# Kernel optimization log

Measured on AMD Instinct MI355X. Metric: run time of the kernel, lower is better.

Reference implementation:

```python
import jax, jax.numpy as jnp
import numpy as np

CHEB_K = 3
HIDDEN = 64
HORIZON = 12
H_FSIZE = 64                      # conv kernel width along the hidden axis
H_FILTER = HORIZON * H_FSIZE      # 768, forced by h.view(N,1,horizon,1,h_filter_size)
N_NODE = 1024
BATCH = 64
T_IN = 12
K2 = (CHEB_K * HIDDEN) ** 2       # 36864, hyp Linear in_features


def setup_inputs() -> dict:
    key = jax.random.key(0)
    k1, k2, k3, k4 = jax.random.split(key, 4)
    output = jax.random.normal(k1, (BATCH, T_IN, N_NODE, HIDDEN), jnp.float32)
    weights = jax.random.normal(k2, (N_NODE, K2), jnp.float32)
    # hyp Linear parameters (torch default init scale ~ 1/sqrt(fan_in))
    W_hyp = jax.random.normal(k3, (H_FILTER, K2), jnp.float32) / np.sqrt(K2).astype(np.float32)
    b_hyp = jax.random.normal(k4, (H_FILTER,), jnp.float32) / np.sqrt(K2).astype(np.float32)
    return {"output": output, "weights": weights, "W_hyp": W_hyp, "b_hyp": b_hyp}


def reference(output, weights, W_hyp, b_hyp):
    B, T, N, D = output.shape
    x = output[:, -1]                              # (B, N, D)   last time step
    w = weights.reshape(N, -1)                     # (N, K2)
    h = w @ W_hyp.T + b_hyp                        # (N, h_filter) hypernet Linear
    h = h.reshape(N, HORIZON, H_FSIZE)             # per-node, per-horizon 1xF filters
    Wout = D - H_FSIZE + 1                         # valid conv width (=1 here)
    # sliding windows of x along D: (B, N, Wout, F)
    idx = jnp.arange(Wout)[:, None] + jnp.arange(H_FSIZE)[None, :]
    xw = x[:, :, idx]
    # grouped conv2d (groups=N, 1 in-ch / horizon out-ch per group) == per-node contraction.
    # The torch sum(dim=3) is over a size-1 axis (no-op). Final layout (B, horizon, N, Wout).
    out = jnp.einsum('bnwf,ntf->btnw', xw, h)
    return out
```

## Files before the change

kernel.cpp:

```cpp
#include <hip/hip_runtime.h>
#include <hip/hip_bf16.h>
#include <cstdint>
#include <cstddef>

#define K2V 36864
#define MN  1024
#define HF  768

typedef __attribute__((ext_vector_type(8))) short short8;
typedef __attribute__((ext_vector_type(4))) float f32x4;

__device__ __forceinline__ unsigned pk_bf2(float a, float b) {
    __hip_bfloat16 ha = __float2bfloat16(a);
    __hip_bfloat16 hb = __float2bfloat16(b);
    unsigned short ua = *reinterpret_cast<unsigned short*>(&ha);
    unsigned short ub = *reinterpret_cast<unsigned short*>(&hb);
    return (unsigned)ua | ((unsigned)ub << 16);
}

__global__ __launch_bounds__(512, 4)
void gemm_h_split(const float* __restrict__ A, const float* __restrict__ B,
                  float* __restrict__ part, int KC)
{
    __shared__ unsigned short sA[2][128 * 64];
    __shared__ unsigned short sB[2][128 * 64];

    const int tid  = threadIdx.x;
    const int lane = tid & 63;
    const int wave = tid >> 6;
    const int wm   = wave >> 2;
    const int wn   = wave & 3;

    int mtile, ntile, kidx;
    if ((gridDim.x & 7) == 0) {
        const int xcd = blockIdx.x & 7;
        const int pos = blockIdx.x >> 3;
        mtile = xcd;
        kidx  = pos / 6;
        ntile = pos - kidx * 6;
    } else {
        kidx = blockIdx.x / 48;
        const int rem = blockIdx.x - kidx * 48;
        mtile = rem / 6;
        ntile = rem - mtile * 6;
    }
    const int k0 = kidx * KC;

    const float* Ap = A + (size_t)(mtile * 128) * K2V + k0;
    const float* Bp = B + (size_t)(ntile * 128) * K2V + k0;

    const int c4 = tid & 15;
    const int r0 = tid >> 4;

    f32x4 acc[4][2];
    #pragma unroll
    for (int i = 0; i < 4; ++i)
        #pragma unroll
        for (int j = 0; j < 2; ++j)
            acc[i][j] = (f32x4){0.f, 0.f, 0.f, 0.f};

    float4 ra[4], rb[4];

    auto load_step = [&](int s) {
        const float* a = Ap + s * 64 + c4 * 4;
        const float* b = Bp + s * 64 + c4 * 4;
        #pragma unroll
        for (int i = 0; i < 4; ++i) {
            const int r = r0 + 32 * i;
            ra[i] = *reinterpret_cast<const float4*>(a + (size_t)r * K2V);
            rb[i] = *reinterpret_cast<const float4*>(b + (size_t)r * K2V);
        }
    };
    auto write_step = [&](int buf) {
        #pragma unroll
        for (int i = 0; i < 4; ++i) {
            const int r = r0 + 32 * i;
            int off = r * 128 + c4 * 8;
            off ^= (r & 7) << 4;
            uint2 va = { pk_bf2(ra[i].x, ra[i].y), pk_bf2(ra[i].z, ra[i].w) };
            uint2 vb = { pk_bf2(rb[i].x, rb[i].y), pk_bf2(rb[i].z, rb[i].w) };
            *reinterpret_cast<uint2*>(reinterpret_cast<char*>(sA[buf]) + off) = va;
            *reinterpret_cast<uint2*>(reinterpret_cast<char*>(sB[buf]) + off) = vb;
        }
    };

    const int nsteps = KC >> 6;

    load_step(0);
    write_step(0);
    __syncthreads();

    for (int s = 0; s < nsteps; ++s) {
        if (s + 1 < nsteps) load_step(s + 1);
        const int buf = s & 1;
        #pragma unroll
        for (int ks = 0; ks < 2; ++ks) {
            short8 av[4], bv[2];
            const int cb = (ks * 32 + (lane >> 4) * 8) * 2;
            #pragma unroll
            for (int i = 0; i < 4; ++i) {
                const int rA = wm * 64 + i * 16 + (lane & 15);
                int oa = rA * 128 + cb; oa ^= (rA & 7) << 4;
                av[i] = *reinterpret_cast<const short8*>(reinterpret_cast<const char*>(sA[buf]) + oa);
            }
            #pragma unroll
            for (int j = 0; j < 2; ++j) {
                const int rB = wn * 32 + j * 16 + (lane & 15);
                int ob = rB * 128 + cb; ob ^= (rB & 7) << 4;
                bv[j] = *reinterpret_cast<const short8*>(reinterpret_cast<const char*>(sB[buf]) + ob);
            }
            #pragma unroll
            for (int i = 0; i < 4; ++i)
                #pragma unroll
                for (int j = 0; j < 2; ++j)
                    acc[i][j] = __builtin_amdgcn_mfma_f32_16x16x32_bf16(av[i], bv[j], acc[i][j], 0, 0, 0);
        }
        if (s + 1 < nsteps) write_step((s + 1) & 1);
        __syncthreads();
    }

    float* P = part + ((size_t)kidx * MN + mtile * 128 + wm * 64) * HF
                    + ntile * 128 + wn * 32;
    #pragma unroll
    for (int i = 0; i < 4; ++i) {
        #pragma unroll
        for (int j = 0; j < 2; ++j) {
            const int col = j * 16 + (lane & 15);
            #pragma unroll
            for (int q = 0; q < 4; ++q) {
                const int row = i * 16 + (lane >> 4) * 4 + q;
                P[(size_t)row * HF + col] = acc[i][j][q];
            }
        }
    }
}

__global__ __launch_bounds__(256)
void h_reduce(float* __restrict__ part, const float* __restrict__ bias, int ksplit)
{
    const int fidx = blockIdx.x * 256 + threadIdx.x;
    const int n  = fidx / 192;
    const int j4 = fidx - n * 192;
    const size_t base = (size_t)n * HF + j4 * 4;
    const size_t kstride = (size_t)MN * HF;

    float4 s0 = *reinterpret_cast<const float4*>(bias + j4 * 4);
    float4 s1 = {0.f, 0.f, 0.f, 0.f}, s2 = {0.f, 0.f, 0.f, 0.f}, s3 = {0.f, 0.f, 0.f, 0.f};
    int k = 0;
    for (; k + 4 <= ksplit; k += 4) {
        float4 p0 = *reinterpret_cast<const float4*>(part + (size_t)(k + 0) * kstride + base);
        float4 p1 = *reinterpret_cast<const float4*>(part + (size_t)(k + 1) * kstride + base);
        float4 p2 = *reinterpret_cast<const float4*>(part + (size_t)(k + 2) * kstride + base);
        float4 p3 = *reinterpret_cast<const float4*>(part + (size_t)(k + 3) * kstride + base);
        s0.x += p0.x; s0.y += p0.y; s0.z += p0.z; s0.w += p0.w;
        s1.x += p1.x; s1.y += p1.y; s1.z += p1.z; s1.w += p1.w;
        s2.x += p2.x; s2.y += p2.y; s2.z += p2.z; s2.w += p2.w;
        s3.x += p3.x; s3.y += p3.y; s3.z += p3.z; s3.w += p3.w;
    }
    for (; k < ksplit; ++k) {
        float4 p0 = *reinterpret_cast<const float4*>(part + (size_t)k * kstride + base);
        s0.x += p0.x; s0.y += p0.y; s0.z += p0.z; s0.w += p0.w;
    }
    float4 r;
    r.x = (s0.x + s1.x) + (s2.x + s3.x);
    r.y = (s0.y + s1.y) + (s2.y + s3.y);
    r.z = (s0.z + s1.z) + (s2.z + s3.z);
    r.w = (s0.w + s1.w) + (s2.w + s3.w);
    *reinterpret_cast<float4*>(part + base) = r;
}

__global__ __launch_bounds__(256)
void hyper_out(const float* __restrict__ xall, const float* __restrict__ hred,
               float* __restrict__ out)
{
    const int n   = blockIdx.x;
    const int tid = threadIdx.x;
    __shared__ float hs[HF];
    __shared__ float xs[64 * 65];

    #pragma unroll
    for (int jj = 0; jj < 3; ++jj) {
        const int j = tid + jj * 256;
        hs[j] = hred[(size_t)n * HF + j];
    }
    {
        const int c4 = tid & 15;
        const int bt = tid >> 4;
        #pragma unroll
        for (int i = 0; i < 4; ++i) {
            const int b = bt + 16 * i;
            const float4 v = *reinterpret_cast<const float4*>(
                xall + ((size_t)(b * 12 + 11) * MN + n) * 64 + c4 * 4);
            xs[b * 65 + c4 * 4 + 0] = v.x;
            xs[b * 65 + c4 * 4 + 1] = v.y;
            xs[b * 65 + c4 * 4 + 2] = v.z;
            xs[b * 65 + c4 * 4 + 3] = v.w;
        }
    }
    __syncthreads();

    const int b  = tid & 63;
    const int t0 = tid >> 6;
    float a0 = 0.f, a1 = 0.f, a2 = 0.f;
    #pragma unroll
    for (int f = 0; f < 64; ++f) {
        const float x = xs[b * 65 + f];
        a0 += x * hs[t0 * 64 + f];
        a1 += x * hs[(t0 + 4) * 64 + f];
        a2 += x * hs[(t0 + 8) * 64 + f];
    }
    out[((size_t)(b * 12 + t0)) * MN + n]     = a0;
    out[((size_t)(b * 12 + t0 + 4)) * MN + n] = a1;
    out[((size_t)(b * 12 + t0 + 8)) * MN + n] = a2;
}

extern "C" void kernel_launch(void* const* d_in, const int* in_sizes, int n_in,
                              void* d_out, int out_size, void* d_ws, size_t ws_size,
                              hipStream_t stream)
{
    const float* xall = (const float*)d_in[0];
    const float* wts  = (const float*)d_in[1];
    const float* Whyp = (const float*)d_in[2];
    const float* bhyp = (const float*)d_in[3];
    float* out  = (float*)d_out;
    float* part = (float*)d_ws;

    const size_t slice = (size_t)MN * HF * sizeof(float);
    int ks = 1;
    const int opts[8] = {16, 12, 8, 6, 4, 3, 2, 1};
    for (int i = 0; i < 8; ++i) {
        if ((size_t)opts[i] * slice <= ws_size) { ks = opts[i]; break; }
    }
    const int KC = K2V / ks;

    gemm_h_split<<<dim3(48 * ks), dim3(512), 0, stream>>>(wts, Whyp, part, KC);
    h_reduce<<<dim3(768), dim3(256), 0, stream>>>(part, bhyp, ks);
    hyper_out<<<dim3(1024), dim3(256), 0, stream>>>(xall, part, out);
}
```

Before: 509.1 us.

## Pre-convert GEMM operands to swizzled bf16 tiles and stream them via global_load_lds

Adds a pre-pass kernel that converts both fp32 GEMM operands into bf16 tiles already laid out in the swizzled LDS order. The main GEMM then copies those tiles straight from global memory into LDS with global_load_lds, double-buffered using explicit waitcnt and barriers. This removes the fp32 register round trip and the in-loop conversion. The cost is an extra full pass that reads all fp32 data and writes it back as bf16, plus a larger workspace, with the old path kept as a fallback when the workspace is too small.

Result: slower. 523.9 us (+2.9%).

```diff
diff --git a/kernel.cpp b/kernel.cpp
--- a/kernel.cpp
+++ b/kernel.cpp
@@ -6,9 +6,14 @@
 #define K2V 36864
 #define MN  1024
 #define HF  768
+#define NKC 576
+#define TILE_SH 8192
 
 typedef __attribute__((ext_vector_type(8))) short short8;
 typedef __attribute__((ext_vector_type(4))) float f32x4;
+
+typedef __attribute__((address_space(3))) void lvoid;
+typedef __attribute__((address_space(1))) const void gvoid;
 
 __device__ __forceinline__ unsigned pk_bf2(float a, float b) {
     __hip_bfloat16 ha = __float2bfloat16(a);
@@ -18,12 +23,49 @@
     return (unsigned)ua | ((unsigned)ub << 16);
 }
 
+__device__ __forceinline__ void gl_lds16(const unsigned short* g, unsigned short* l) {
+    __builtin_amdgcn_global_load_lds((gvoid*)g, (lvoid*)l, 16, 0, 0);
+}
+
+__global__ __launch_bounds__(256)
+void convert_tiles(const float* __restrict__ A, const float* __restrict__ B,
+                   unsigned short* __restrict__ dst)
+{
+    const int b = blockIdx.x;
+    const float* src;
+    unsigned short* out;
+    if (b < 8 * NKC) {
+        const int mt = b / NKC, kc = b - mt * NKC;
+        src = A + (size_t)(mt * 128) * K2V + kc * 64;
+        out = dst + (size_t)b * TILE_SH;
+    } else {
+        const int bb = b - 8 * NKC;
+        const int nt = bb / NKC, kc = bb - nt * NKC;
+        src = B + (size_t)(nt * 128) * K2V + kc * 64;
+        out = dst + (size_t)b * TILE_SH;
+    }
+    const int c8 = threadIdx.x & 7;
+    const int r0 = threadIdx.x >> 3;
+    #pragma unroll
+    for (int i = 0; i < 4; ++i) {
+        const int r = r0 + 32 * i;
+        const float* p = src + (size_t)r * K2V + c8 * 8;
+        const float4 v0 = *reinterpret_cast<const float4*>(p);
+        const float4 v1 = *reinterpret_cast<const float4*>(p + 4);
+        uint4 w = { pk_bf2(v0.x, v0.y), pk_bf2(v0.z, v0.w),
+                    pk_bf2(v1.x, v1.y), pk_bf2(v1.z, v1.w) };
+        const int off = (r * 128 + c8 * 16) ^ ((r & 7) << 4);
+        *reinterpret_cast<uint4*>(reinterpret_cast<char*>(out) + off) = w;
+    }
+}
+
 __global__ __launch_bounds__(512, 4)
-void gemm_h_split(const float* __restrict__ A, const float* __restrict__ B,
-                  float* __restrict__ part, int KC)
-{
-    __shared__ unsigned short sA[2][128 * 64];
-    __shared__ unsigned short sB[2][128 * 64];
+void gemm_bf16(const unsigned short* __restrict__ Abf,
+               const unsigned short* __restrict__ Bbf,
+               float* __restrict__ part, int NSTEP)
+{
+    __shared__ unsigned short sA[2][TILE_SH];
+    __shared__ unsigned short sB[2][TILE_SH];
 
     const int tid  = threadIdx.x;
     const int lane = tid & 63;
@@ -33,9 +75,8 @@
 
     int mtile, ntile, kidx;
     if ((gridDim.x & 7) == 0) {
-        const int xcd = blockIdx.x & 7;
+        mtile = blockIdx.x & 7;
         const int pos = blockIdx.x >> 3;
-        mtile = xcd;
         kidx  = pos / 6;
         ntile = pos - kidx * 6;
     } else {
@@ -44,6 +85,117 @@
         mtile = rem / 6;
         ntile = rem - mtile * 6;
     }
+
+    const unsigned short* At = Abf + ((size_t)mtile * NKC + kidx * NSTEP) * TILE_SH;
+    const unsigned short* Bt = Bbf + ((size_t)ntile * NKC + kidx * NSTEP) * TILE_SH;
+
+    f32x4 acc[4][2];
+    #pragma unroll
+    for (int i = 0; i < 4; ++i)
+        #pragma unroll
+        for (int j = 0; j < 2; ++j)
+            acc[i][j] = (f32x4){0.f, 0.f, 0.f, 0.f};
+
+    auto stage = [&](int s, int buf) {
+        const unsigned short* ga = At + (size_t)s * TILE_SH + tid * 8;
+        const unsigned short* gb = Bt + (size_t)s * TILE_SH + tid * 8;
+        gl_lds16(ga,        &sA[buf][tid * 8]);
+        gl_lds16(ga + 4096, &sA[buf][4096 + tid * 8]);
+        gl_lds16(gb,        &sB[buf][tid * 8]);
+        gl_lds16(gb + 4096, &sB[buf][4096 + tid * 8]);
+    };
+
+    auto compute = [&](int buf) {
+        #pragma unroll
+        for (int ks = 0; ks < 2; ++ks) {
+            short8 av[4], bv[2];
+            const int cb = (ks * 32 + (lane >> 4) * 8) * 2;
+            #pragma unroll
+            for (int i = 0; i < 4; ++i) {
+                const int rA = wm * 64 + i * 16 + (lane & 15);
+                const int oa = (rA * 128 + cb) ^ ((rA & 7) << 4);
+                av[i] = *reinterpret_cast<const short8*>(
+                          reinterpret_cast<const char*>(sA[buf]) + oa);
+            }
+            #pragma unroll
+            for (int j = 0; j < 2; ++j) {
+                const int rB = wn * 32 + j * 16 + (lane & 15);
+                const int ob = (rB * 128 + cb) ^ ((rB & 7) << 4);
+                bv[j] = *reinterpret_cast<const short8*>(
+                          reinterpret_cast<const char*>(sB[buf]) + ob);
+            }
+            #pragma unroll
+            for (int i = 0; i < 4; ++i)
+                #pragma unroll
+                for (int j = 0; j < 2; ++j)
+                    acc[i][j] = __builtin_amdgcn_mfma_f32_16x16x32_bf16(av[i], bv[j], acc[i][j], 0, 0, 0);
+        }
+    };
+
+    stage(0, 0);
+    stage(1, 1);
+    asm volatile("s_waitcnt vmcnt(4)" ::: "memory");
+    __builtin_amdgcn_s_barrier();
+
+    for (int s = 0; s < NSTEP - 2; ++s) {
+        const int buf = s & 1;
+        compute(buf);
+        asm volatile("s_waitcnt lgkmcnt(0)" ::: "memory");
+        __builtin_amdgcn_s_barrier();
+        stage(s + 2, buf);
+        asm volatile("s_waitcnt vmcnt(4)" ::: "memory");
+        __builtin_amdgcn_s_barrier();
+    }
+    {
+        compute((NSTEP - 2) & 1);
+        asm volatile("s_waitcnt lgkmcnt(0)" ::: "memory");
+        __builtin_amdgcn_s_barrier();
+        asm volatile("s_waitcnt vmcnt(0)" ::: "memory");
+        __builtin_amdgcn_s_barrier();
+        compute((NSTEP - 1) & 1);
+    }
+
+    float* P = part + ((size_t)kidx * MN + mtile * 128 + wm * 64) * HF
+                    + ntile * 128 + wn * 32;
+    #pragma unroll
+    for (int i = 0; i < 4; ++i) {
+        #pragma unroll
+        for (int j = 0; j < 2; ++j) {
+            const int col = j * 16 + (lane & 15);
+            #pragma unroll
+            for (int q = 0; q < 4; ++q) {
+                const int row = i * 16 + (lane >> 4) * 4 + q;
+                P[(size_t)row * HF + col] = acc[i][j][q];
+            }
+        }
+    }
+}
+
+__global__ __launch_bounds__(512, 4)
+void gemm_h_split(const float* __restrict__ A, const float* __restrict__ B,
+                  float* __restrict__ part, int KC)
+{
+    __shared__ unsigned short sA[2][128 * 64];
+    __shared__ unsigned short sB[2][128 * 64];
+
+    const int tid  = threadIdx.x;
+    const int lane = tid & 63;
+    const int wave = tid >> 6;
+    const int wm   = wave >> 2;
+    const int wn   = wave & 3;
+
+    int mtile, ntile, kidx;
+    if ((gridDim.x & 7) == 0) {
+        mtile = blockIdx.x & 7;
+        const int pos = blockIdx.x >> 3;
+        kidx  = pos / 6;
+        ntile = pos - kidx * 6;
+    } else {
+        kidx = blockIdx.x / 48;
+        const int rem = blockIdx.x - kidx * 48;
+        mtile = rem / 6;
+        ntile = rem - mtile * 6;
+    }
     const int k0 = kidx * KC;
 
     const float* Ap = A + (size_t)(mtile * 128) * K2V + k0;
@@ -60,7 +212,6 @@
             acc[i][j] = (f32x4){0.f, 0.f, 0.f, 0.f};
 
     float4 ra[4], rb[4];
-
     auto load_step = [&](int s) {
         const float* a = Ap + s * 64 + c4 * 4;
         const float* b = Bp + s * 64 + c4 * 4;
@@ -85,7 +236,6 @@
     };
 
     const int nsteps = KC >> 6;
-
     load_step(0);
     write_step(0);
     __syncthreads();
@@ -145,7 +295,7 @@
     const size_t kstride = (size_t)MN * HF;
 
     float4 s0 = *reinterpret_cast<const float4*>(bias + j4 * 4);
-    float4 s1 = {0.f, 0.f, 0.f, 0.f}, s2 = {0.f, 0.f, 0.f, 0.f}, s3 = {0.f, 0.f, 0.f, 0.f};
+    float4 s1 = {0.f,0.f,0.f,0.f}, s2 = {0.f,0.f,0.f,0.f}, s3 = {0.f,0.f,0.f,0.f};
     int k = 0;
     for (; k + 4 <= ksplit; k += 4) {
         float4 p0 = *reinterpret_cast<const float4*>(part + (size_t)(k + 0) * kstride + base);
@@ -222,18 +372,34 @@
     const float* wts  = (const float*)d_in[1];
     const float* Whyp = (const float*)d_in[2];
     const float* bhyp = (const float*)d_in[3];
-    float* out  = (float*)d_out;
-    float* part = (float*)d_ws;
-
-    const size_t slice = (size_t)MN * HF * sizeof(float);
-    int ks = 1;
+    float* out = (float*)d_out;
+
+    const size_t slice  = (size_t)MN * HF * sizeof(float);
+    const size_t bf_sz  = (size_t)(8 + 6) * NKC * TILE_SH * 2;
     const int opts[8] = {16, 12, 8, 6, 4, 3, 2, 1};
-    for (int i = 0; i < 8; ++i) {
-        if ((size_t)opts[i] * slice <= ws_size) { ks = opts[i]; break; }
-    }
-    const int KC = K2V / ks;
-
-    gemm_h_split<<<dim3(48 * ks), dim3(512), 0, stream>>>(wts, Whyp, part, KC);
-    h_reduce<<<dim3(768), dim3(256), 0, stream>>>(part, bhyp, ks);
-    hyper_out<<<dim3(1024), dim3(256), 0, stream>>>(xall, part, out);
-}
+
+    int ks_bf = 0;
+    for (int i = 0; i < 8; ++i)
+        if (bf_sz + (size_t)opts[i] * slice <= ws_size) { ks_bf = opts[i]; break; }
+
+    if (ks_bf >= 4) {
+        unsigned short* tiles = (unsigned short*)d_ws;
+        unsigned short* Bbf   = tiles + (size_t)8 * NKC * TILE_SH;
+        float* part = (float*)((char*)d_ws + bf_sz);
+        const int NSTEP = NKC / ks_bf;
+
+        convert_tiles<<<dim3(14 * NKC), dim3(256), 0, stream>>>(wts, Whyp, tiles);
+        gemm_bf16<<<dim3(48 * ks_bf), dim3(512), 0, stream>>>(tiles, Bbf, part, NSTEP);
+        h_reduce<<<dim3(768), dim3(256), 0, stream>>>(part, bhyp, ks_bf);
+        hyper_out<<<dim3(1024), dim3(256), 0, stream>>>(xall, part, out);
+    } else {
+        float* part = (float*)d_ws;
+        int ks = 1;
+        for (int i = 0; i < 8; ++i)
+            if ((size_t)opts[i] * slice <= ws_size) { ks = opts[i]; break; }
+        const int KC = K2V / ks;
+        gemm_h_split<<<dim3(48 * ks), dim3(512), 0, stream>>>(wts, Whyp, part, KC);
+        h_reduce<<<dim3(768), dim3(256), 0, stream>>>(part, bhyp, ks);
+        hyper_out<<<dim3(1024), dim3(256), 0, stream>>>(xall, part, out);
+    }
+}
```
